# Kernel optimization log

Hardware: AMD Instinct MI355X
Metric: run time of the kernel (lower is better)

Reference implementation:

```python
import jax, jax.numpy as jnp
import numpy as np

N = 50000
E = 500000
NODE_F = 128
POS_F = 3
COORD_F = 64
EDGE_IN = 2 * NODE_F + 1  # 257


def _linear_params(key, fan_in, fan_out):
    k1, k2 = jax.random.split(key)
    bound = 1.0 / np.sqrt(fan_in)
    W = jax.random.uniform(k1, (fan_in, fan_out), jnp.float32, -bound, bound)
    b = jax.random.uniform(k2, (fan_out,), jnp.float32, -bound, bound)
    return W, b


def setup_inputs() -> dict:
    key = jax.random.key(0)
    ks = jax.random.split(key, 8)
    x = jax.random.normal(ks[0], (N, NODE_F + POS_F), jnp.float32)
    edge_index = jax.random.randint(ks[1], (2, E), 0, N, jnp.int64)
    W_e1, b_e1 = _linear_params(ks[2], EDGE_IN, 2 * EDGE_IN)
    W_e2, b_e2 = _linear_params(ks[3], 2 * EDGE_IN, COORD_F)
    W_c1, b_c1 = _linear_params(ks[4], COORD_F, 4 * COORD_F)
    W_c2, b_c2 = _linear_params(ks[5], 4 * COORD_F, 1)
    W_n1, b_n1 = _linear_params(ks[6], NODE_F + COORD_F, 2 * NODE_F)
    W_n2, b_n2 = _linear_params(ks[7], 2 * NODE_F, NODE_F)
    return {"x": x, "edge_index": edge_index,
            "W_e1": W_e1, "b_e1": b_e1, "W_e2": W_e2, "b_e2": b_e2,
            "W_c1": W_c1, "b_c1": b_c1, "W_c2": W_c2, "b_c2": b_c2,
            "W_n1": W_n1, "b_n1": b_n1, "W_n2": W_n2, "b_n2": b_n2}


def reference(x, edge_index, W_e1, b_e1, W_e2, b_e2, W_c1, b_c1, W_c2, b_c2,
              W_n1, b_n1, W_n2, b_n2):
    node = x[:, :-POS_F]            # (N, 128)
    coords = x[:, -POS_F:]          # (N, 3)
    src = edge_index[0]             # j (source)
    dst = edge_index[1]             # i (target)

    rel_coords = coords[src] - coords[dst]                          # (E, 3)
    rel_dist = jnp.sqrt(jnp.sum(rel_coords ** 2, -1, keepdims=True))  # (E, 1)

    # message: edge_mlp(cat[x_i, x_j, edge_attr])
    e_in = jnp.concatenate([node[dst], node[src], rel_dist], axis=-1)  # (E, 257)
    h = jax.nn.silu(e_in @ W_e1 + b_e1)
    m_ij = jax.nn.silu(h @ W_e2 + b_e2)                             # (E, 64)
    coord_w = jax.nn.silu(m_ij @ W_c1 + b_c1) @ W_c2 + b_c2         # (E, 1)

    # scatter-sum aggregation to target nodes
    m_i = jax.ops.segment_sum(m_ij, dst, num_segments=N)            # (N, 64)
    w_i = jax.ops.segment_sum(coord_w, dst, num_segments=N)         # (N, 1)
    r_i = jax.ops.segment_sum(rel_coords, dst, num_segments=N)      # (N, 3)

    coords_out = coords + w_i * r_i
    n_in = jnp.concatenate([node, m_i], axis=-1)                    # (N, 192)
    hidden = jax.nn.silu(n_in @ W_n1 + b_n1) @ W_n2 + b_n2 + node   # (N, 128)
    return jnp.concatenate([hidden, coords_out], axis=-1)           # (N, 131)
```

## Files before the change

kernel.cpp:

```cpp
#include <hip/hip_runtime.h>
#include <hip/hip_bf16.h>
#include <hip/hip_fp16.h>

#define NN 50000
#define NE 500000
#define DCAP 48

using bf16x8 = __attribute__((ext_vector_type(8))) short;
using f16x8  = __attribute__((ext_vector_type(8))) _Float16;
using f32x4  = __attribute__((ext_vector_type(4))) float;
using f32x2  = __attribute__((ext_vector_type(2))) float;

__device__ __forceinline__ float b2f(unsigned short s) {
  union { unsigned u; float f; } v; v.u = ((unsigned)s) << 16; return v.f;
}
__device__ __forceinline__ unsigned short f2b(float f) {
  __hip_bfloat16 h = __float2bfloat16(f);
  return *reinterpret_cast<unsigned short*>(&h);
}
__device__ __forceinline__ unsigned short f2h(float f) {
  __half h = __float2half(f);
  return *reinterpret_cast<unsigned short*>(&h);
}
__device__ __forceinline__ float hu2f(unsigned short s) {
  __half h; *reinterpret_cast<unsigned short*>(&h) = s; return __half2float(h);
}
__device__ __forceinline__ unsigned pack2(float a, float b) {
  __hip_bfloat162 h = __float22bfloat162_rn(make_float2(a, b));
  return *reinterpret_cast<unsigned*>(&h);
}
__device__ __forceinline__ unsigned pack2h(float a, float b) {
  __half2 h = __float22half2_rn(make_float2(a, b));
  return *reinterpret_cast<unsigned*>(&h);
}
__device__ __forceinline__ __half2 h2u(unsigned u) {
  union { unsigned v; __half2 h; } x; x.v = u; return x.h;
}
__device__ __forceinline__ unsigned u2h(__half2 h) {
  union { __half2 h; unsigned v; } x; x.h = h; return x.v;
}
__device__ __forceinline__ float silu_f(float x) {
  return x * __builtin_amdgcn_rcpf(1.f + __expf(-x));
}
__device__ __forceinline__ __half2 silu2(__half2 z) {
  const __half2 one = __float2half2_rn(1.f);
  __half2 e = h2exp(__hneg2(z));
  return __hmul2(z, h2rcp(__hadd2(e, one)));
}

#define WPREP 269344
#define B0 (WPREP + NN * 17)
#define B1 (B0 + NN)
#define B2 (B1 + 1)
#define B3 (B2 + NE)
#define B4 (B3 + NN * 16)
#define PREP_TOTAL (B4 + NN)
__global__ void prep_all(const float* __restrict__ we1,
                         const float* __restrict__ be1,
                         const float* __restrict__ we2,
                         const float* __restrict__ be2,
                         const float* __restrict__ wc1,
                         const float* __restrict__ wn1,
                         const float* __restrict__ wn2,
                         const float* __restrict__ x,
                         unsigned short* __restrict__ A1p,
                         unsigned short* __restrict__ A2p,
                         unsigned short* __restrict__ AdB,
                         unsigned short* __restrict__ W2p,
                         unsigned short* __restrict__ Wc1p,
                         unsigned short* __restrict__ Wn1p,
                         unsigned short* __restrict__ Wn2p,
                         float* __restrict__ be1p,
                         unsigned short* __restrict__ node_p,
                         float* __restrict__ coords_p,
                         int* __restrict__ cnt,
                         int* __restrict__ total,
                         int* __restrict__ esrc,
                         float* __restrict__ m_i,
                         float* __restrict__ wr) {
  int i = blockIdx.x * 256 + threadIdx.x;
  if (i < 67584) {
    int n = i / 128, k = i % 128;
    A1p[i] = (n < 514) ? f2b(we1[k * 514 + n]) : (unsigned short)0;
  } else if (i < 135168) {
    int j = i - 67584; int n = j / 128, k = j % 128;
    A2p[j] = (n < 514) ? f2b(we1[(128 + k) * 514 + n]) : (unsigned short)0;
  } else if (i < 135696) {
    int j = i - 135168;
    AdB[j] = (j < 514) ? f2h(we1[256 * 514 + j]) : (unsigned short)0;
  } else if (i < 170512) {
    int j = i - 135696; int n = j / 544, lk = j % 544;
    unsigned short v = 0;
    if (lk < 514) v = f2h(we2[lk * 64 + n]);
    else if (lk == 514) v = f2h(be2[n]);
    W2p[j] = v;
  } else if (i < 186896) {
    int j = i - 170512; int n = j / 64, k = j % 64;
    Wc1p[j] = f2b(wc1[k * 256 + n]);
  } else if (i < 236048) {
    int j = i - 186896; int n = j / 192, k = j % 192;
    Wn1p[j] = f2b(wn1[k * 256 + n]);
  } else if (i < 268816) {
    int j = i - 236048; int n = j / 256, k = j % 256;
    Wn2p[j] = f2b(wn2[k * 128 + n]);
  } else if (i < WPREP) {
    int j = i - 268816;
    be1p[j] = (j < 514) ? be1[j] : 0.f;
  } else if (i < B0) {
    int j = i - WPREP;
    if (j < NN * 16) {
      int g = j >> 4, c = j & 15;
      const float* s = x + g * 131 + c * 8;
      unsigned short* d = node_p + g * 128 + c * 8;
#pragma unroll
      for (int q = 0; q < 8; q++) d[q] = f2b(s[q]);
    } else {
      int g = j - NN * 16;
      float4 c;
      c.x = x[g * 131 + 128];
      c.y = x[g * 131 + 129];
      c.z = x[g * 131 + 130];
      c.w = 0.f;
      *(float4*)(coords_p + g * 4) = c;
    }
  } else if (i < B1) {
    cnt[i - B0] = 0;
  } else if (i < B2) {
    total[0] = 0;
  } else if (i < B3) {
    esrc[i - B2] = -1;
  } else if (i < B4) {
    int j = i - B3;
    *(float4*)(m_i + (size_t)j * 4) = make_float4(0.f, 0.f, 0.f, 0.f);
  } else if (i < PREP_TOTAL) {
    int j = i - B4;
    *(float4*)(wr + j * 4) = make_float4(0.f, 0.f, 0.f, 0.f);
  }
}

__global__ void build_adj(const int* __restrict__ eidx,
                          int* __restrict__ cnt, int* __restrict__ adj) {
  int e = blockIdx.x * 256 + threadIdx.x;
  if (e < NE) {
    int d = eidx[NE + e];
    d = min(max(d, 0), NN - 1);
    int slot = atomicAdd(&cnt[d], 1);
    if (slot < DCAP) adj[d * DCAP + slot] = e;
  }
}

__global__ void assign_off(const int* __restrict__ cnt,
                           int* __restrict__ off,
                           int* __restrict__ total) {
  int g = blockIdx.x * 256 + threadIdx.x;
  int lane = threadIdx.x & 63;
  int deg = (g < NN) ? min(cnt[g], DCAP) : 0;
  int incl = deg;
#pragma unroll
  for (int d = 1; d < 64; d <<= 1) {
    int v = __shfl_up(incl, d, 64);
    if (lane >= d) incl += v;
  }
  int wsum = __shfl(incl, 63, 64);
  int base = 0;
  if (lane == 63) base = atomicAdd(total, wsum);
  base = __shfl(base, 63, 64);
  if (g < NN) off[g] = base + incl - deg;
}

__global__ void compact_adj(const int* __restrict__ cnt,
                            const int* __restrict__ off,
                            const int* __restrict__ adj,
                            const int* __restrict__ eidx,
                            const float* __restrict__ coords_p,
                            int* __restrict__ esrc,
                            int* __restrict__ edst,
                            float* __restrict__ scoord) {
  int t = blockIdx.x * 256 + threadIdx.x;
  if (t >= NN * DCAP) return;
  int g = t / DCAP, k = t % DCAP;
  int deg = min(cnt[g], DCAP);
  if (k >= deg) return;
  int e = adj[t];
  int s = eidx[e];
  s = min(max(s, 0), NN - 1);
  int o = off[g] + k;
  esrc[o] = s;
  edst[o] = g;
  float4 cs = *(const float4*)(coords_p + s * 4);
  float4 cd = *(const float4*)(coords_p + g * 4);
  float rx = cs.x - cd.x, ry = cs.y - cd.y, rz = cs.z - cd.z;
  float4 sc;
  sc.x = rx; sc.y = ry; sc.z = rz;
  sc.w = sqrtf(rx * rx + ry * ry + rz * rz);
  *(float4*)(scoord + (size_t)o * 4) = sc;
}

__launch_bounds__(256, 2)
__global__ void pgemm_kernel(const unsigned short* __restrict__ node_p,
                             const unsigned short* __restrict__ A1p,
                             const unsigned short* __restrict__ A2p,
                             const float* __restrict__ be1p,
                             unsigned short* __restrict__ P1,
                             unsigned char* __restrict__ P2) {
  __shared__ unsigned short sNode[64][136];
  int tid = threadIdx.x, blk = blockIdx.x;
  int lane = tid & 63, wv = tid >> 6, l16 = lane & 15, quad = lane >> 4;
#pragma unroll
  for (int it = 0; it < 4; it++) {
    int t = tid + it * 256;
    int row = t >> 4, ch = t & 15;
    int g = blk * 64 + row;
    if (g >= NN) g = 0;
    *(bf16x8*)(&sNode[row][ch * 8]) = *(const bf16x8*)(node_p + g * 128 + ch * 8);
  }
  __syncthreads();
#pragma unroll 1
  for (int t = 0; t < 9; t++) {
    int T = wv + 4 * t;
    if (T >= 33) break;
    f32x4 a1[4], a2[4];
#pragma unroll
    for (int s = 0; s < 4; s++) {
      a1[s] = (f32x4){0.f, 0.f, 0.f, 0.f};
      a2[s] = (f32x4){0.f, 0.f, 0.f, 0.f};
    }
    for (int kb = 0; kb < 4; kb++) {
      bf16x8 b1 = *(const bf16x8*)(A1p + (T * 16 + l16) * 128 + kb * 32 + quad * 8);
      bf16x8 b2 = *(const bf16x8*)(A2p + (T * 16 + l16) * 128 + kb * 32 + quad * 8);
#pragma unroll
      for (int s = 0; s < 4; s++) {
        bf16x8 a = *(const bf16x8*)(&sNode[s * 16 + l16][kb * 32 + quad * 8]);
        a1[s] = __builtin_amdgcn_mfma_f32_16x16x32_bf16(b1, a, a1[s], 0, 0, 0);
        a2[s] = __builtin_amdgcn_mfma_f32_16x16x32_bf16(b2, a, a2[s], 0, 0, 0);
      }
    }
    int nb = T * 16 + quad * 4;
    float4 b4 = *(const float4*)(be1p + nb);
    bool v0 = nb + 0 < 514, v1 = nb + 1 < 514, v2 = nb + 2 < 514, v3 = nb + 3 < 514;
#pragma unroll
    for (int s = 0; s < 4; s++) {
      int g = blk * 64 + s * 16 + l16;
      if (g < NN) {
        float p0 = v0 ? a1[s][0] + b4.x : 0.f;
        float p1v = v1 ? a1[s][1] + b4.y : 0.f;
        float p2v = v2 ? a1[s][2] + b4.z : 0.f;
        float p3 = v3 ? a1[s][3] + b4.w : 0.f;
        *(uint2*)(P1 + g * 528 + nb) = make_uint2(pack2h(p0, p1v), pack2h(p2v, p3));
        float q0 = v0 ? a2[s][0] : 0.f;
        float q1 = v1 ? a2[s][1] : 0.f;
        float q2 = v2 ? a2[s][2] : 0.f;
        float q3 = v3 ? a2[s][3] : 0.f;
        int w8 = __builtin_amdgcn_cvt_pk_fp8_f32(q0, q1, 0, false);
        w8 = __builtin_amdgcn_cvt_pk_fp8_f32(q2, q3, w8, true);
        *(unsigned*)(P2 + g * 528 + nb) = (unsigned)w8;
      }
    }
  }
}

__launch_bounds__(256, 3)
__global__ void edge_kernel(const unsigned short* __restrict__ P1,
                            const unsigned char* __restrict__ P2,
                            const unsigned short* __restrict__ AdB,
                            const int* __restrict__ esrcA,
                            const int* __restrict__ edstA,
                            const float* __restrict__ scoord,
                            const unsigned short* __restrict__ W2p,
                            const unsigned short* __restrict__ Wc1p,
                            const float* __restrict__ bc1,
                            const float* __restrict__ bc2,
                            const float* __restrict__ wc2,
                            float* __restrict__ m_i,
                            float* __restrict__ wr) {
  __shared__ unsigned short sHc[48][168];
  __shared__ unsigned short sM[48][72];
  __shared__ int sDst[48];
  __shared__ int sSrc[48];
  __shared__ int sE[48];
  __shared__ float sDistF[48];
  __shared__ float sCwPart[4][48];
  int tid = threadIdx.x, blk = blockIdx.x;
  int lane = tid & 63, wv = tid >> 6, l16 = lane & 15, quad = lane >> 4;

  unsigned tailP1 = 0u, tailP2 = 0u;
  if (tid < 48) {
    int r = blk * 48 + tid;
    int s = (r < NE) ? esrcA[r] : -1;
    sE[tid] = s;
    int ss = (s < 0) ? 0 : s;
    int d = 0;
    float dist = 0.f;
    if (s >= 0) {
      d = edstA[r];
      d = min(max(d, 0), NN - 1);
      dist = scoord[(size_t)r * 4 + 3];
    }
    sDst[tid] = d;
    sSrc[tid] = ss;
    sDistF[tid] = dist;
    tailP1 = *(const unsigned*)(P1 + d * 528 + 512);
    tailP2 = *(const unsigned*)(P2 + ss * 528 + 512);
  }
  __syncthreads();

  int cg = tid & 15, er = tid >> 4;
  const unsigned short* p1b[3];
  const unsigned char* p2b[3];
  __half2 d2[3];
#pragma unroll
  for (int it = 0; it < 3; it++) {
    int edge = er + it * 16;
    p1b[it] = P1 + sDst[edge] * 528 + cg * 8;
    p2b[it] = P2 + sSrc[edge] * 528 + cg * 8;
    d2[it] = __float2half2_rn(sDistF[edge]);
  }
  const unsigned short* adB = AdB + cg * 8;
  const unsigned short* w2b = W2p + (wv * 16 + l16) * 544 + quad * 8;

  uint2 u2r[4][3];
#pragma unroll
  for (int ch = 0; ch < 4; ch++)
#pragma unroll
    for (int it = 0; it < 3; it++)
      u2r[ch][it] = *(const uint2*)(p2b[it] + ch * 128);

  f32x4 macc[3];
#pragma unroll
  for (int s = 0; s < 3; s++) macc[s] = (f32x4){0.f, 0.f, 0.f, 0.f};

#pragma unroll
  for (int ch = 0; ch < 4; ch++) {
    uint4 uva = *(const uint4*)(adB + ch * 128);
    __half2 va0 = h2u(uva.x), va1 = h2u(uva.y), va2 = h2u(uva.z), va3 = h2u(uva.w);
#pragma unroll
    for (int it = 0; it < 3; it++) {
      int edge = er + it * 16;
      uint4 u1 = *(const uint4*)(p1b[it] + ch * 128);
      uint2 u2 = u2r[ch][it];
      f32x2 c0 = __builtin_amdgcn_cvt_pk_f32_fp8((int)u2.x, false);
      f32x2 c1 = __builtin_amdgcn_cvt_pk_f32_fp8((int)u2.x, true);
      f32x2 c2 = __builtin_amdgcn_cvt_pk_f32_fp8((int)u2.y, false);
      f32x2 c3 = __builtin_amdgcn_cvt_pk_f32_fp8((int)u2.y, true);
      __half2 q0 = h2u(pack2h(c0.x, c0.y));
      __half2 q1 = h2u(pack2h(c1.x, c1.y));
      __half2 q2 = h2u(pack2h(c2.x, c2.y));
      __half2 q3 = h2u(pack2h(c3.x, c3.y));
      __half2 z0 = __hfma2(va0, d2[it], __hadd2(h2u(u1.x), q0));
      __half2 z1 = __hfma2(va1, d2[it], __hadd2(h2u(u1.y), q1));
      __half2 z2 = __hfma2(va2, d2[it], __hadd2(h2u(u1.z), q2));
      __half2 z3 = __hfma2(va3, d2[it], __hadd2(h2u(u1.w), q3));
      *(uint4*)(&sHc[edge][cg * 8]) = make_uint4(
          u2h(silu2(z0)), u2h(silu2(z1)), u2h(silu2(z2)), u2h(silu2(z3)));
    }
    if (ch == 3 && tid < 48) {
      float dist = sDistF[tid];
      __half2 hp1 = h2u(tailP1);
      f32x2 t2 = __builtin_amdgcn_cvt_pk_f32_fp8((int)tailP2, false);
      float h512 = silu_f(__low2float(hp1) + t2.x + dist * hu2f(AdB[512]));
      float h513 = silu_f(__high2float(hp1) + t2.y + dist * hu2f(AdB[513]));
      *(uint4*)(&sHc[tid][128]) = make_uint4(pack2h(h512, h513), pack2h(1.0f, 0.f), 0u, 0u);
      *(uint4*)(&sHc[tid][136]) = make_uint4(0u, 0u, 0u, 0u);
      *(uint4*)(&sHc[tid][144]) = make_uint4(0u, 0u, 0u, 0u);
      *(uint4*)(&sHc[tid][152]) = make_uint4(0u, 0u, 0u, 0u);
    }
    __syncthreads();
    const int nkb = (ch == 3) ? 5 : 4;
#pragma unroll
    for (int kb = 0; kb < nkb; kb++) {
      f16x8 b = *(const f16x8*)(w2b + ch * 128 + kb * 32);
#pragma unroll
      for (int s = 0; s < 3; s++) {
        f16x8 a = *(const f16x8*)(&sHc[s * 16 + l16][kb * 32 + quad * 8]);
        macc[s] = __builtin_amdgcn_mfma_f32_16x16x32_f16(b, a, macc[s], 0, 0, 0);
      }
    }
    __syncthreads();
  }

  {
    int nb = wv * 16 + quad * 4;
#pragma unroll
    for (int s = 0; s < 3; s++) {
      unsigned lo = pack2(silu_f(macc[s][0]), silu_f(macc[s][1]));
      unsigned hi = pack2(silu_f(macc[s][2]), silu_f(macc[s][3]));
      *(uint2*)(&sM[s * 16 + l16][nb]) = make_uint2(lo, hi);
    }
  }
  __syncthreads();

  {
    float cw[3] = {0.f, 0.f, 0.f};
#pragma unroll
    for (int jt = 0; jt < 4; jt++) {
      int T = wv * 4 + jt;
      f32x4 cacc[3];
#pragma unroll
      for (int s = 0; s < 3; s++) cacc[s] = (f32x4){0.f, 0.f, 0.f, 0.f};
#pragma unroll
      for (int kb = 0; kb < 2; kb++) {
        bf16x8 b = *(const bf16x8*)(Wc1p + (T * 16 + l16) * 64 + kb * 32 + quad * 8);
#pragma unroll
        for (int s = 0; s < 3; s++) {
          bf16x8 a = *(const bf16x8*)(&sM[s * 16 + l16][kb * 32 + quad * 8]);
          cacc[s] = __builtin_amdgcn_mfma_f32_16x16x32_bf16(b, a, cacc[s], 0, 0, 0);
        }
      }
      int nb = T * 16 + quad * 4;
      float4 b4 = *(const float4*)(bc1 + nb);
      float4 w4 = *(const float4*)(wc2 + nb);
#pragma unroll
      for (int s = 0; s < 3; s++) {
        cw[s] += silu_f(cacc[s][0] + b4.x) * w4.x;
        cw[s] += silu_f(cacc[s][1] + b4.y) * w4.y;
        cw[s] += silu_f(cacc[s][2] + b4.z) * w4.z;
        cw[s] += silu_f(cacc[s][3] + b4.w) * w4.w;
      }
    }
#pragma unroll
    for (int s = 0; s < 3; s++) {
      cw[s] += __shfl_xor(cw[s], 16, 64);
      cw[s] += __shfl_xor(cw[s], 32, 64);
    }
    if (quad == 0) {
#pragma unroll
      for (int s = 0; s < 3; s++) sCwPart[wv][s * 16 + l16] = cw[s];
    }
  }
  __syncthreads();

  {
    int c = tid & 63, q = tid >> 6;
    float acc = 0.f; int cur = -1;
#pragma unroll
    for (int e0 = 0; e0 < 12; e0++) {
      int e = q * 12 + e0;
      if (sE[e] < 0) continue;
      int d = sDst[e];
      float v = b2f(sM[e][c]);
      if (d != cur) {
        if (cur >= 0) atomicAdd(&m_i[(size_t)cur * 64 + c], acc);
        cur = d; acc = v;
      } else {
        acc += v;
      }
    }
    if (cur >= 0) atomicAdd(&m_i[(size_t)cur * 64 + c], acc);
  }
  if (tid < 192) {
    int e = tid >> 2, comp = tid & 3;
    if (sE[e] >= 0) {
      int r = blk * 48 + e;
      int d = sDst[e];
      float val;
      if (comp == 3)
        val = sCwPart[0][e] + sCwPart[1][e] + sCwPart[2][e] + sCwPart[3][e]
              + bc2[0];
      else
        val = scoord[(size_t)r * 4 + comp];
      atomicAdd(&wr[d * 4 + comp], val);
    }
  }
}

__launch_bounds__(256, 2)
__global__ void node_mlp_kernel(const unsigned short* __restrict__ node_p,
                                const float* __restrict__ x,
                                const float* __restrict__ coords_p,
                                const float* __restrict__ m_i,
                                const float* __restrict__ wr,
                                const unsigned short* __restrict__ Wn1p,
                                const unsigned short* __restrict__ Wn2p,
                                const float* __restrict__ bn1,
                                const float* __restrict__ bn2,
                                float* __restrict__ out) {
  __shared__ unsigned short sNin[64][200];
  __shared__ unsigned short sHid[64][264];
  __shared__ float sWr[64][4];
  int tid = threadIdx.x, blk = blockIdx.x;
  int lane = tid & 63, wv = tid >> 6, l16 = lane & 15, quad = lane >> 4;

#pragma unroll
  for (int it = 0; it < 4; it++) {
    int t = tid + it * 256;
    int row = t >> 4, ch = t & 15;
    int g = blk * 64 + row;
    if (g >= NN) g = 0;
    *(bf16x8*)(&sNin[row][ch * 8]) = *(const bf16x8*)(node_p + g * 128 + ch * 8);
  }
  {
    int row = tid >> 2, c = tid & 3;
    int g = blk * 64 + row;
    int gg = (g < NN) ? g : 0;
    const float4* mi = (const float4*)(m_i + (size_t)gg * 64 + c * 16);
    float4 v1 = mi[0], v2 = mi[1], v3 = mi[2], v4 = mi[3];
    *(uint4*)(&sNin[row][128 + c * 16]) = make_uint4(
        pack2(v1.x, v1.y), pack2(v1.z, v1.w), pack2(v2.x, v2.y), pack2(v2.z, v2.w));
    *(uint4*)(&sNin[row][128 + c * 16 + 8]) = make_uint4(
        pack2(v3.x, v3.y), pack2(v3.z, v3.w), pack2(v4.x, v4.y), pack2(v4.z, v4.w));
    sWr[row][c] = wr[gg * 4 + c];
  }
  __syncthreads();
  {
    f32x4 acc[4][4];
#pragma unroll
    for (int j = 0; j < 4; j++)
#pragma unroll
      for (int s = 0; s < 4; s++) acc[j][s] = (f32x4){0.f, 0.f, 0.f, 0.f};
    for (int kb = 0; kb < 6; kb++) {
      bf16x8 afr[4], bfr[4];
#pragma unroll
      for (int s = 0; s < 4; s++)
        afr[s] = *(const bf16x8*)(&sNin[s * 16 + l16][kb * 32 + quad * 8]);
#pragma unroll
      for (int j = 0; j < 4; j++)
        bfr[j] = *(const bf16x8*)(Wn1p + ((wv * 4 + j) * 16 + l16) * 192 + kb * 32 + quad * 8);
#pragma unroll
      for (int j = 0; j < 4; j++)
#pragma unroll
        for (int s = 0; s < 4; s++)
          acc[j][s] = __builtin_amdgcn_mfma_f32_16x16x32_bf16(bfr[j], afr[s], acc[j][s], 0, 0, 0);
    }
#pragma unroll
    for (int j = 0; j < 4; j++) {
      int nb = (wv * 4 + j) * 16 + quad * 4;
      float4 b4 = *(const float4*)(bn1 + nb);
#pragma unroll
      for (int s = 0; s < 4; s++) {
        unsigned lo = pack2(silu_f(acc[j][s][0] + b4.x), silu_f(acc[j][s][1] + b4.y));
        unsigned hi = pack2(silu_f(acc[j][s][2] + b4.z), silu_f(acc[j][s][3] + b4.w));
        *(uint2*)(&sHid[s * 16 + l16][nb]) = make_uint2(lo, hi);
      }
    }
  }
  __syncthreads();
  {
    f32x4 acc[2][4];
#pragma unroll
    for (int j = 0; j < 2; j++)
#pragma unroll
      for (int s = 0; s < 4; s++) acc[j][s] = (f32x4){0.f, 0.f, 0.f, 0.f};
    for (int kb = 0; kb < 8; kb++) {
      bf16x8 afr[4], bfr[2];
#pragma unroll
      for (int s = 0; s < 4; s++)
        afr[s] = *(const bf16x8*)(&sHid[s * 16 + l16][kb * 32 + quad * 8]);
#pragma unroll
      for (int j = 0; j < 2; j++)
        bfr[j] = *(const bf16x8*)(Wn2p + ((wv * 2 + j) * 16 + l16) * 256 + kb * 32 + quad * 8);
#pragma unroll
      for (int j = 0; j < 2; j++)
#pragma unroll
        for (int s = 0; s < 4; s++)
          acc[j][s] = __builtin_amdgcn_mfma_f32_16x16x32_bf16(bfr[j], afr[s], acc[j][s], 0, 0, 0);
    }
#pragma unroll
    for (int j = 0; j < 2; j++) {
      int nb = (wv * 2 + j) * 16 + quad * 4;
      float4 b4 = *(const float4*)(bn2 + nb);
#pragma unroll
      for (int s = 0; s < 4; s++) {
        int g = blk * 64 + s * 16 + l16;
        if (g < NN) {
          int base = g * 131 + nb;
          out[base + 0] = acc[j][s][0] + b4.x + x[base + 0];
          out[base + 1] = acc[j][s][1] + b4.y + x[base + 1];
          out[base + 2] = acc[j][s][2] + b4.z + x[base + 2];
          out[base + 3] = acc[j][s][3] + b4.w + x[base + 3];
        }
      }
    }
  }
  if (tid < 64) {
    int g = blk * 64 + tid;
    if (g < NN) {
      float w = sWr[tid][3];
      out[g * 131 + 128] = coords_p[g * 4 + 0] + w * sWr[tid][0];
      out[g * 131 + 129] = coords_p[g * 4 + 1] + w * sWr[tid][1];
      out[g * 131 + 130] = coords_p[g * 4 + 2] + w * sWr[tid][2];
    }
  }
}

extern "C" void kernel_launch(void* const* d_in, const int* in_sizes, int n_in,
                              void* d_out, int out_size, void* d_ws, size_t ws_size,
                              hipStream_t stream) {
  const float* x   = (const float*)d_in[0];
  const int* eidx  = (const int*)d_in[1];
  const float* we1 = (const float*)d_in[2];
  const float* be1 = (const float*)d_in[3];
  const float* we2 = (const float*)d_in[4];
  const float* be2 = (const float*)d_in[5];
  const float* wc1 = (const float*)d_in[6];
  const float* bc1 = (const float*)d_in[7];
  const float* wc2 = (const float*)d_in[8];
  const float* bc2 = (const float*)d_in[9];
  const float* wn1 = (const float*)d_in[10];
  const float* bn1 = (const float*)d_in[11];
  const float* wn2 = (const float*)d_in[12];
  const float* bn2 = (const float*)d_in[13];

  char* ws = (char*)d_ws;
  unsigned short* A1p    = (unsigned short*)(ws + 0);
  unsigned short* A2p    = (unsigned short*)(ws + 135168);
  unsigned short* AdB    = (unsigned short*)(ws + 270336);
  unsigned short* W2p    = (unsigned short*)(ws + 271392);
  unsigned short* Wc1p   = (unsigned short*)(ws + 341024);
  unsigned short* Wn1p   = (unsigned short*)(ws + 373792);
  unsigned short* Wn2p   = (unsigned short*)(ws + 472096);
  float* be1p            = (float*)(ws + 537632);
  unsigned short* node_p = (unsigned short*)(ws + 539744);
  float* coords_p        = (float*)(ws + 13339744);
  float* m_i             = (float*)(ws + 14139744);
  float* wr              = (float*)(ws + 78139744);
  int* cnt               = (int*)(ws + 80139744);
  int* adj               = (int*)(ws + 80339744);
  unsigned short* P1     = (unsigned short*)(ws + 103539744);
  unsigned char* P2      = (unsigned char*)(ws + 156339744);
  int* off               = (int*)(ws + 209139744);
  int* edst              = (int*)(ws + 209339748);
  int* esrc              = (int*)(ws + 211339748);
  int* total             = (int*)(ws + 213339748);
  float* scoord          = (float*)(ws + 213339760);

  prep_all<<<(PREP_TOTAL + 255) / 256, 256, 0, stream>>>(
      we1, be1, we2, be2, wc1, wn1, wn2, x,
      A1p, A2p, AdB, W2p, Wc1p, Wn1p, Wn2p, be1p, node_p, coords_p,
      cnt, total, esrc, m_i, wr);
  pgemm_kernel<<<(NN + 63) / 64, 256, 0, stream>>>(node_p, A1p, A2p, be1p, P1, P2);
  build_adj<<<(NE + 255) / 256, 256, 0, stream>>>(eidx, cnt, adj);
  assign_off<<<(NN + 255) / 256, 256, 0, stream>>>(cnt, off, total);
  compact_adj<<<(NN * DCAP + 255) / 256, 256, 0, stream>>>(cnt, off, adj, eidx,
                                                           coords_p, esrc, edst,
                                                           scoord);
  edge_kernel<<<(NE + 47) / 48, 256, 0, stream>>>(P1, P2, AdB, esrc, edst, scoord,
                                                  W2p, Wc1p, bc1, bc2, wc2,
                                                  m_i, wr);
  node_mlp_kernel<<<(NN + 63) / 64, 256, 0, stream>>>(node_p, x, coords_p, m_i, wr,
                                                      Wn1p, Wn2p, bn1, bn2,
                                                      (float*)d_out);
}
```

Before: 414.5 us.

## Double-buffer edge hidden chunks to overlap combine with MFMA

Splits the shared hidden-activation buffer into two alternating buffers. Each chunk's gather/combine/silu now runs while the MFMAs consume the previous chunk, so only one barrier is needed per chunk instead of two. The goal is to overlap the global gathers and VALU work with matrix ops and to cut synchronisation. It adds about 13 KB more LDS per block, which may lower occupancy under launch_bounds(256,3).

```diff
diff --git a/kernel.cpp b/kernel.cpp
--- a/kernel.cpp
+++ b/kernel.cpp
@@ -259,6 +259,45 @@
   }
 }
 
+#define COMBINE_CH(CHX, BUF, PITCH)                                           \
+  {                                                                           \
+    uint4 uva = *(const uint4*)(adB + (CHX) * 128);                           \
+    __half2 va0 = h2u(uva.x), va1 = h2u(uva.y), va2 = h2u(uva.z),             \
+            va3 = h2u(uva.w);                                                 \
+    _Pragma("unroll")                                                         \
+    for (int it = 0; it < 3; it++) {                                          \
+      int edge = er + it * 16;                                                \
+      uint4 u1 = *(const uint4*)(p1b[it] + (CHX) * 128);                      \
+      uint2 u2 = u2r[CHX][it];                                                \
+      f32x2 c0 = __builtin_amdgcn_cvt_pk_f32_fp8((int)u2.x, false);           \
+      f32x2 c1 = __builtin_amdgcn_cvt_pk_f32_fp8((int)u2.x, true);            \
+      f32x2 c2 = __builtin_amdgcn_cvt_pk_f32_fp8((int)u2.y, false);           \
+      f32x2 c3 = __builtin_amdgcn_cvt_pk_f32_fp8((int)u2.y, true);            \
+      __half2 q0 = h2u(pack2h(c0.x, c0.y));                                   \
+      __half2 q1 = h2u(pack2h(c1.x, c1.y));                                   \
+      __half2 q2 = h2u(pack2h(c2.x, c2.y));                                   \
+      __half2 q3 = h2u(pack2h(c3.x, c3.y));                                   \
+      __half2 z0 = __hfma2(va0, d2[it], __hadd2(h2u(u1.x), q0));              \
+      __half2 z1 = __hfma2(va1, d2[it], __hadd2(h2u(u1.y), q1));              \
+      __half2 z2 = __hfma2(va2, d2[it], __hadd2(h2u(u1.z), q2));              \
+      __half2 z3 = __hfma2(va3, d2[it], __hadd2(h2u(u1.w), q3));              \
+      *(uint4*)((BUF) + edge * (PITCH) + cg * 8) = make_uint4(                \
+          u2h(silu2(z0)), u2h(silu2(z1)), u2h(silu2(z2)), u2h(silu2(z3)));    \
+    }                                                                         \
+  }
+
+#define MFMA_CH(CHX, BUF, PITCH, NKB)                                         \
+  _Pragma("unroll")                                                           \
+  for (int kb = 0; kb < (NKB); kb++) {                                        \
+    f16x8 b = *(const f16x8*)(w2b + (CHX) * 128 + kb * 32);                   \
+    _Pragma("unroll")                                                         \
+    for (int s = 0; s < 3; s++) {                                             \
+      f16x8 a = *(const f16x8*)((BUF) + (s * 16 + l16) * (PITCH) + kb * 32 +  \
+                                quad * 8);                                    \
+      macc[s] = __builtin_amdgcn_mfma_f32_16x16x32_f16(b, a, macc[s], 0, 0, 0); \
+    }                                                                         \
+  }
+
 __launch_bounds__(256, 3)
 __global__ void edge_kernel(const unsigned short* __restrict__ P1,
                             const unsigned char* __restrict__ P2,
@@ -273,7 +312,8 @@
                             const float* __restrict__ wc2,
                             float* __restrict__ m_i,
                             float* __restrict__ wr) {
-  __shared__ unsigned short sHc[48][168];
+  __shared__ unsigned short sHcA[48][136];
+  __shared__ unsigned short sHcB[48][168];
   __shared__ unsigned short sM[48][72];
   __shared__ int sDst[48];
   __shared__ int sSrc[48];
@@ -329,54 +369,38 @@
 #pragma unroll
   for (int s = 0; s < 3; s++) macc[s] = (f32x4){0.f, 0.f, 0.f, 0.f};
 
-#pragma unroll
-  for (int ch = 0; ch < 4; ch++) {
-    uint4 uva = *(const uint4*)(adB + ch * 128);
-    __half2 va0 = h2u(uva.x), va1 = h2u(uva.y), va2 = h2u(uva.z), va3 = h2u(uva.w);
-#pragma unroll
-    for (int it = 0; it < 3; it++) {
-      int edge = er + it * 16;
-      uint4 u1 = *(const uint4*)(p1b[it] + ch * 128);
-      uint2 u2 = u2r[ch][it];
-      f32x2 c0 = __builtin_amdgcn_cvt_pk_f32_fp8((int)u2.x, false);
-      f32x2 c1 = __builtin_amdgcn_cvt_pk_f32_fp8((int)u2.x, true);
-      f32x2 c2 = __builtin_amdgcn_cvt_pk_f32_fp8((int)u2.y, false);
-      f32x2 c3 = __builtin_amdgcn_cvt_pk_f32_fp8((int)u2.y, true);
-      __half2 q0 = h2u(pack2h(c0.x, c0.y));
-      __half2 q1 = h2u(pack2h(c1.x, c1.y));
-      __half2 q2 = h2u(pack2h(c2.x, c2.y));
-      __half2 q3 = h2u(pack2h(c3.x, c3.y));
-      __half2 z0 = __hfma2(va0, d2[it], __hadd2(h2u(u1.x), q0));
-      __half2 z1 = __hfma2(va1, d2[it], __hadd2(h2u(u1.y), q1));
-      __half2 z2 = __hfma2(va2, d2[it], __hadd2(h2u(u1.z), q2));
-      __half2 z3 = __hfma2(va3, d2[it], __hadd2(h2u(u1.w), q3));
-      *(uint4*)(&sHc[edge][cg * 8]) = make_uint4(
-          u2h(silu2(z0)), u2h(silu2(z1)), u2h(silu2(z2)), u2h(silu2(z3)));
-    }
-    if (ch == 3 && tid < 48) {
-      float dist = sDistF[tid];
-      __half2 hp1 = h2u(tailP1);
-      f32x2 t2 = __builtin_amdgcn_cvt_pk_f32_fp8((int)tailP2, false);
-      float h512 = silu_f(__low2float(hp1) + t2.x + dist * hu2f(AdB[512]));
-      float h513 = silu_f(__high2float(hp1) + t2.y + dist * hu2f(AdB[513]));
-      *(uint4*)(&sHc[tid][128]) = make_uint4(pack2h(h512, h513), pack2h(1.0f, 0.f), 0u, 0u);
-      *(uint4*)(&sHc[tid][136]) = make_uint4(0u, 0u, 0u, 0u);
-      *(uint4*)(&sHc[tid][144]) = make_uint4(0u, 0u, 0u, 0u);
-      *(uint4*)(&sHc[tid][152]) = make_uint4(0u, 0u, 0u, 0u);
-    }
-    __syncthreads();
-    const int nkb = (ch == 3) ? 5 : 4;
-#pragma unroll
-    for (int kb = 0; kb < nkb; kb++) {
-      f16x8 b = *(const f16x8*)(w2b + ch * 128 + kb * 32);
-#pragma unroll
-      for (int s = 0; s < 3; s++) {
-        f16x8 a = *(const f16x8*)(&sHc[s * 16 + l16][kb * 32 + quad * 8]);
-        macc[s] = __builtin_amdgcn_mfma_f32_16x16x32_f16(b, a, macc[s], 0, 0, 0);
-      }
-    }
-    __syncthreads();
-  }
+  unsigned short* bufA = &sHcA[0][0];
+  unsigned short* bufB = &sHcB[0][0];
+
+  COMBINE_CH(0, bufA, 136);
+  __syncthreads();
+
+  COMBINE_CH(1, bufB, 168);
+  MFMA_CH(0, bufA, 136, 4);
+  __syncthreads();
+
+  COMBINE_CH(2, bufA, 136);
+  MFMA_CH(1, bufB, 168, 4);
+  __syncthreads();
+
+  COMBINE_CH(3, bufB, 168);
+  if (tid < 48) {
+    float dist = sDistF[tid];
+    __half2 hp1 = h2u(tailP1);
+    f32x2 t2 = __builtin_amdgcn_cvt_pk_f32_fp8((int)tailP2, false);
+    float h512 = silu_f(__low2float(hp1) + t2.x + dist * hu2f(AdB[512]));
+    float h513 = silu_f(__high2float(hp1) + t2.y + dist * hu2f(AdB[513]));
+    unsigned short* tb = bufB + tid * 168;
+    *(uint4*)(tb + 128) = make_uint4(pack2h(h512, h513), pack2h(1.0f, 0.f), 0u, 0u);
+    *(uint4*)(tb + 136) = make_uint4(0u, 0u, 0u, 0u);
+    *(uint4*)(tb + 144) = make_uint4(0u, 0u, 0u, 0u);
+    *(uint4*)(tb + 152) = make_uint4(0u, 0u, 0u, 0u);
+  }
+  MFMA_CH(2, bufA, 136, 4);
+  __syncthreads();
+
+  MFMA_CH(3, bufB, 168, 5);
+  __syncthreads();
 
   {
     int nb = wv * 16 + quad * 4;
```

After: 423.1 us. +2.1%, slower.
